# Optimization experiments

Hardware: AMD Instinct MI355X
Metric: run time of the kernel (lower is better)

The kernel has to match this reference:

```python
import jax, jax.numpy as jnp
import numpy as np

B, T, E, H, D = 1, 2048, 1024, 16, 64  # H*D == E required by module


def setup_inputs() -> dict:
    key = jax.random.key(0)
    ks = jax.random.split(key, 9)
    s_in = (2.0 / E) ** 0.5
    return {
        "x": jax.random.normal(ks[0], (B, T, E), jnp.float32),
        "wq": jax.random.normal(ks[1], (H * D, E), jnp.float32) * E ** -0.5,
        "wk": jax.random.normal(ks[2], (H * D, E), jnp.float32) * E ** -0.5,
        "wv": jax.random.normal(ks[3], (H * D, E), jnp.float32) * E ** -0.5,
        "wr": jax.random.normal(ks[4], (H, E, T), jnp.float32) * s_in,
        "wvr": jax.random.normal(ks[5], (H * D, E), jnp.float32) * E ** -0.5,
        "wj": jax.random.normal(ks[6], (E, E), jnp.float32) * E ** -0.5,
        "gate": jnp.zeros((H, 3), jnp.float32),
        "wo": jax.random.normal(ks[7], (E, H * D), jnp.float32) * E ** -0.5,
    }


def reference(x, wq, wk, wv, wr, wvr, wj, gate, wo):
    Bx, Tx, Ex = x.shape
    Hh = wr.shape[0]
    Dd = wq.shape[0] // Hh
    scale = 1.0 / Dd ** 0.5
    neg = -jnp.inf
    mask = jnp.triu(jnp.ones((Tx, Tx), bool), 1)  # True above diagonal

    def heads(w):  # (B,T,H*D) -> (B,H,T,D)
        return (x @ w.T).reshape(Bx, Tx, Hh, Dd).transpose(0, 2, 1, 3)

    # --- branch 1: standard causal QKV attention ---
    q, k, v = heads(wq), heads(wk), heads(wv)
    qkv_attn = jnp.einsum('bhqd,bhkd->bhqk', q, k) * scale
    qkv_attn = jnp.where(mask, neg, qkv_attn)
    qkv_out = jnp.einsum('bhqk,bhkd->bhqd', jax.nn.softmax(qkv_attn, axis=-1), v)

    # --- branch 2: RRPRAM learned per-position scores ---
    rv = heads(wvr)
    r = jnp.einsum('bte,het->bht', x, wr[:, :, :Tx])  # (B,H,T) key scores
    r_attn = jnp.where(mask, neg, (r * scale)[:, :, None, :])  # (B,H,T,T)
    rrp_out = jnp.einsum('bhqk,bhkd->bhqd', jax.nn.softmax(r_attn, axis=-1), rv)

    # --- branch 3: Janus self-resonance ---
    echo = x @ wj.T            # (B,T,E)
    echo_back = echo @ wj      # F.linear(echo, wj.weight.T)
    scores = (x * echo_back).sum(-1) / Ex ** 0.5  # (B,T)
    j_attn = jnp.where(mask, neg, scores[:, :, None] * scores[:, None, :])  # (B,T,T)
    jA = jax.nn.softmax(j_attn, axis=-1)
    j_val = echo.reshape(Bx, Tx, Hh, Dd).transpose(0, 2, 1, 3)
    jan_out = jnp.einsum('bqk,bhkd->bhqd', jA, j_val)

    # --- gated combine + output proj ---
    g = jax.nn.softmax(gate, axis=-1)  # (H,3)
    out = (g[:, 0][None, :, None, None] * qkv_out
           + g[:, 1][None, :, None, None] * rrp_out
           + g[:, 2][None, :, None, None] * jan_out)
    out = out.transpose(0, 2, 1, 3).reshape(Bx, Tx, Hh * Dd)
    return out @ wo.T
```

## Files before the change

### kernel.cpp

```cpp
#include <hip/hip_runtime.h>
#include <cstddef>
#include <cstdint>

#define TT 2048
#define EE 1024
#define HH 16
#define NSP 4

typedef unsigned short ushort;
typedef unsigned int uint;
typedef __attribute__((ext_vector_type(8))) short short8;
typedef __attribute__((ext_vector_type(8))) _Float16 half8;
typedef __attribute__((ext_vector_type(4))) float f32x4;
typedef __attribute__((ext_vector_type(4))) ushort ushort4v;

__device__ __forceinline__ ushort f2bf(float f) {
  uint u = __builtin_bit_cast(uint, f);
  u = (u + 0x7FFFu + ((u >> 16) & 1u)) >> 16;
  return (ushort)u;
}
__device__ __forceinline__ float bf2f(ushort h) {
  return __builtin_bit_cast(float, (uint)h << 16);
}

__device__ __forceinline__ void async16(ushort* lds, const ushort* g) {
  __builtin_amdgcn_global_load_lds(
      reinterpret_cast<const __attribute__((address_space(1))) void*>(
          reinterpret_cast<uintptr_t>(g)),
      reinterpret_cast<__attribute__((address_space(3))) void*>(
          static_cast<unsigned int>(reinterpret_cast<uintptr_t>(lds))),
      16, 0, 0);
}

__global__ __launch_bounds__(256) void cvt_x_k(
    const float* __restrict__ in, ushort* __restrict__ obf,
    ushort* __restrict__ oh, float* __restrict__ snorm, int n) {
  if (blockIdx.x == 0) {
    for (int i = threadIdx.x; i < TT; i += 256) snorm[i] = 0.f;
  }
  int i = (blockIdx.x * 256 + threadIdx.x) * 4;
  if (i >= n) return;
  float4 v = *(const float4*)(in + i);
  ushort4v b, h;
  b.x = f2bf(v.x); b.y = f2bf(v.y); b.z = f2bf(v.z); b.w = f2bf(v.w);
  h.x = __builtin_bit_cast(ushort, (_Float16)v.x);
  h.y = __builtin_bit_cast(ushort, (_Float16)v.y);
  h.z = __builtin_bit_cast(ushort, (_Float16)v.z);
  h.w = __builtin_bit_cast(ushort, (_Float16)v.w);
  *(ushort4v*)(obf + i) = b;
  *(ushort4v*)(oh + i) = h;
}

__global__ __launch_bounds__(256) void cvt_w_k(
    const float* __restrict__ s0, const float* __restrict__ s1,
    const float* __restrict__ s2, const float* __restrict__ s3,
    const float* __restrict__ s4, const float* __restrict__ s5,
    ushort* __restrict__ d0, ushort* __restrict__ d1,
    ushort* __restrict__ d2, ushort* __restrict__ d3,
    ushort* __restrict__ d4, ushort* __restrict__ d5, int n) {
  const int which = blockIdx.y;
  const float* src; ushort* dst;
  switch (which) {
    case 0: src = s0; dst = d0; break;
    case 1: src = s1; dst = d1; break;
    case 2: src = s2; dst = d2; break;
    case 3: src = s3; dst = d3; break;
    case 4: src = s4; dst = d4; break;
    default: src = s5; dst = d5; break;
  }
  int i = (blockIdx.x * 256 + threadIdx.x) * 4;
  if (i >= n) return;
  float4 v = *(const float4*)(src + i);
  ushort4v o;
  if (which == 5) {
    o.x = __builtin_bit_cast(ushort, (_Float16)v.x);
    o.y = __builtin_bit_cast(ushort, (_Float16)v.y);
    o.z = __builtin_bit_cast(ushort, (_Float16)v.z);
    o.w = __builtin_bit_cast(ushort, (_Float16)v.w);
  } else {
    o.x = f2bf(v.x); o.y = f2bf(v.y); o.z = f2bf(v.z); o.w = f2bf(v.w);
  }
  *(ushort4v*)(dst + i) = o;
}

__global__ __launch_bounds__(256) void transpose_k(
    const float* __restrict__ in, float* __restrict__ outT, int M, int N)
{
  __shared__ float tile[32][33];
  const int bn = blockIdx.x * 32;
  const int bm = blockIdx.y * 32;
  const int tx = threadIdx.x & 31, ty = threadIdx.x >> 5;
#pragma unroll
  for (int i = 0; i < 32; i += 8)
    tile[ty + i][tx] = in[(size_t)(bm + ty + i) * N + bn + tx];
  __syncthreads();
#pragma unroll
  for (int i = 0; i < 32; i += 8)
    outT[(size_t)(bn + ty + i) * M + bm + tx] = tile[tx][ty + i];
}

__global__ __launch_bounds__(256) void proj5(
    const ushort* __restrict__ Abf, const ushort* __restrict__ Ah,
    const ushort* __restrict__ B0, const ushort* __restrict__ B1,
    const ushort* __restrict__ B2, const ushort* __restrict__ B3,
    const ushort* __restrict__ B4,
    ushort* __restrict__ C0, ushort* __restrict__ C1,
    ushort* __restrict__ C2, ushort* __restrict__ C3,
    ushort* __restrict__ C4, float* __restrict__ snorm,
    int M, int N, int K)
{
  const ushort* A; const ushort* B; ushort* C; int om;
  switch (blockIdx.z) {
    case 0: A = Abf; B = B0; C = C0; om = 1; break;
    case 1: A = Abf; B = B1; C = C1; om = 1; break;
    case 2: A = Abf; B = B2; C = C2; om = 2; break;
    case 3: A = Abf; B = B3; C = C3; om = 1; break;
    default: A = Ah; B = B4; C = C4; om = 3; break;
  }
  const bool f16 = (blockIdx.z == 4);
  __shared__ __align__(16) ushort As[2][128 * 64];
  __shared__ __align__(16) ushort Bs[2][128 * 64];
  const int tid = threadIdx.x;
  const int m0 = blockIdx.y * 128, n0 = blockIdx.x * 128;
  const int w = tid >> 6, lane = tid & 63;
  const int wr = w >> 1, wc = w & 1;
  const int lr = lane & 15, lk = lane >> 4;
  const int srow = lane >> 3;
  const int scol = ((lane & 7) ^ srow) * 8;
  const ushort* AgL = A + (size_t)(m0 + w * 32 + srow) * K + scol;
  const ushort* BgL = B + (size_t)(n0 + w * 32 + srow) * K + scol;
  const int sbase = (w * 32) * 64;
  const int s0 = (lk ^ (lr & 7)) * 8;
  f32x4 acc[4][4] = {};
  const int NT = K >> 6;
#pragma unroll
  for (int c = 0; c < 4; ++c) {
    async16(&As[0][sbase + c * 8 * 64], AgL + (size_t)c * 8 * K);
    async16(&Bs[0][sbase + c * 8 * 64], BgL + (size_t)c * 8 * K);
  }
  __syncthreads();
  for (int kt = 0; kt < NT; ++kt) {
    const int cur = kt & 1;
    if (kt + 1 < NT) {
      const int kn = (kt + 1) << 6;
#pragma unroll
      for (int c = 0; c < 4; ++c) {
        async16(&As[cur ^ 1][sbase + c * 8 * 64], AgL + (size_t)c * 8 * K + kn);
        async16(&Bs[cur ^ 1][sbase + c * 8 * 64], BgL + (size_t)c * 8 * K + kn);
      }
    }
    short8 a0[4], a1[4], b0[4], b1[4];
#pragma unroll
    for (int i = 0; i < 4; ++i) {
      const ushort* p = &As[cur][(wr * 64 + i * 16 + lr) * 64];
      a0[i] = *(const short8*)(p + s0);
      a1[i] = *(const short8*)(p + (s0 ^ 32));
    }
#pragma unroll
    for (int j = 0; j < 4; ++j) {
      const ushort* p = &Bs[cur][(wc * 64 + j * 16 + lr) * 64];
      b0[j] = *(const short8*)(p + s0);
      b1[j] = *(const short8*)(p + (s0 ^ 32));
    }
    if (f16) {
#pragma unroll
      for (int i = 0; i < 4; ++i)
#pragma unroll
        for (int j = 0; j < 4; ++j) {
          acc[i][j] = __builtin_amdgcn_mfma_f32_16x16x32_f16(
              __builtin_bit_cast(half8, a0[i]), __builtin_bit_cast(half8, b0[j]),
              acc[i][j], 0, 0, 0);
          acc[i][j] = __builtin_amdgcn_mfma_f32_16x16x32_f16(
              __builtin_bit_cast(half8, a1[i]), __builtin_bit_cast(half8, b1[j]),
              acc[i][j], 0, 0, 0);
        }
    } else {
#pragma unroll
      for (int i = 0; i < 4; ++i)
#pragma unroll
        for (int j = 0; j < 4; ++j) {
          acc[i][j] = __builtin_amdgcn_mfma_f32_16x16x32_bf16(
              a0[i], b0[j], acc[i][j], 0, 0, 0);
          acc[i][j] = __builtin_amdgcn_mfma_f32_16x16x32_bf16(
              a1[i], b1[j], acc[i][j], 0, 0, 0);
        }
    }
    __syncthreads();
  }
#pragma unroll
  for (int i = 0; i < 4; ++i)
#pragma unroll
    for (int r = 0; r < 4; ++r) {
      int row = m0 + wr * 64 + i * 16 + lk * 4 + r;
#pragma unroll
      for (int j = 0; j < 4; ++j) {
        int col = n0 + wc * 64 + j * 16 + lr;
        ushort v = f2bf(acc[i][j][r]);
        if (om == 1)
          C[((size_t)(col >> 6) * M + row) * 64 + (col & 63)] = v;
        else if (om == 2)
          C[(size_t)(col >> 6) * 64 * M + (size_t)(col & 63) * M + row] = v;
        else
          C[(size_t)col * M + row] = v;
      }
    }
  if (om == 3) {
#pragma unroll
    for (int i = 0; i < 4; ++i)
#pragma unroll
      for (int r = 0; r < 4; ++r) {
        float p = 0.f;
#pragma unroll
        for (int j = 0; j < 4; ++j) p += acc[i][j][r] * acc[i][j][r];
        p += __shfl_xor(p, 1); p += __shfl_xor(p, 2);
        p += __shfl_xor(p, 4); p += __shfl_xor(p, 8);
        if (lr == 0)
          atomicAdd(&snorm[m0 + wr * 64 + i * 16 + lk * 4 + r], p);
      }
  }
}

template<bool CZ>
__global__ __launch_bounds__(256) void gemm_mfma(
    const ushort* __restrict__ A, const ushort* __restrict__ B,
    float* __restrict__ Cp, int M, int N, int K)
{
  __shared__ __align__(16) ushort As[2][128 * 64];
  __shared__ __align__(16) ushort Bs[2][128 * 64];
  const int tid = threadIdx.x;
  const int m0 = blockIdx.y * 128, n0 = blockIdx.x * 128;
  const int w = tid >> 6, lane = tid & 63;
  const int wr = w >> 1, wc = w & 1;
  const int lr = lane & 15, lk = lane >> 4;
  const int srow = lane >> 3;
  const int scol = ((lane & 7) ^ srow) * 8;
  const ushort* AgL = A + (size_t)(m0 + w * 32 + srow) * K + scol;
  const ushort* BgL = B + (size_t)(n0 + w * 32 + srow) * K + scol;
  const int sbase = (w * 32) * 64;
  const int s0 = (lk ^ (lr & 7)) * 8;
  f32x4 acc[4][4] = {};
  const int Keff = CZ ? (K < m0 + 128 ? K : m0 + 128) : K;
  const int NT = Keff >> 6;
#pragma unroll
  for (int c = 0; c < 4; ++c) {
    async16(&As[0][sbase + c * 8 * 64], AgL + (size_t)c * 8 * K);
    async16(&Bs[0][sbase + c * 8 * 64], BgL + (size_t)c * 8 * K);
  }
  __syncthreads();
  for (int kt = 0; kt < NT; ++kt) {
    const int cur = kt & 1;
    if (kt + 1 < NT) {
      const int kn = (kt + 1) << 6;
#pragma unroll
      for (int c = 0; c < 4; ++c) {
        async16(&As[cur ^ 1][sbase + c * 8 * 64], AgL + (size_t)c * 8 * K + kn);
        async16(&Bs[cur ^ 1][sbase + c * 8 * 64], BgL + (size_t)c * 8 * K + kn);
      }
    }
    short8 a0[4], a1[4], b0[4], b1[4];
#pragma unroll
    for (int i = 0; i < 4; ++i) {
      const ushort* p = &As[cur][(wr * 64 + i * 16 + lr) * 64];
      a0[i] = *(const short8*)(p + s0);
      a1[i] = *(const short8*)(p + (s0 ^ 32));
    }
#pragma unroll
    for (int j = 0; j < 4; ++j) {
      const ushort* p = &Bs[cur][(wc * 64 + j * 16 + lr) * 64];
      b0[j] = *(const short8*)(p + s0);
      b1[j] = *(const short8*)(p + (s0 ^ 32));
    }
#pragma unroll
    for (int i = 0; i < 4; ++i)
#pragma unroll
      for (int j = 0; j < 4; ++j) {
        acc[i][j] = __builtin_amdgcn_mfma_f32_16x16x32_bf16(
            a0[i], b0[j], acc[i][j], 0, 0, 0);
        acc[i][j] = __builtin_amdgcn_mfma_f32_16x16x32_bf16(
            a1[i], b1[j], acc[i][j], 0, 0, 0);
      }
    __syncthreads();
  }
#pragma unroll
  for (int i = 0; i < 4; ++i)
#pragma unroll
    for (int r = 0; r < 4; ++r) {
      int row = m0 + wr * 64 + i * 16 + lk * 4 + r;
#pragma unroll
      for (int j = 0; j < 4; ++j) {
        int col = n0 + wc * 64 + j * 16 + lr;
        Cp[(size_t)row * N + col] = acc[i][j][r];
      }
    }
}

__global__ __launch_bounds__(256) void flash_mfma(
    const ushort* __restrict__ Qg, const ushort* __restrict__ Kg,
    const ushort* __restrict__ Vg, float* __restrict__ pbuf, int T, int nqt)
{
  const int bid = blockIdx.x;
  const int xcd = bid & 7;
  const int jj = bid >> 3;
  const int h = xcd * 2 + (jj & 1);
  const int rest = jj >> 1;
  const int sp = rest & 3;
  const int qt = (nqt - 1) - (rest >> 2);
  const int q0 = qt * 64;
  const int nk = qt + 1;
  const int span = (nk + NSP - 1) >> 2;
  const int kb = sp * span;
  const int ke = (nk < kb + span) ? nk : (kb + span);
  const int tid = threadIdx.x, w = tid >> 6, lane = tid & 63;
  const int lr = lane & 15, lk = lane >> 4;
  const ushort* Q = Qg + (size_t)h * T * 64;
  const ushort* K = Kg + (size_t)h * T * 64;
  const ushort* V = Vg + (size_t)h * 64 * T;
  __shared__ __align__(16) ushort Ps[4][16 * 72];
  const float CEXP = 0.18033688f;

  f32x4 o[4] = {};
  float ls[4] = {0.f, 0.f, 0.f, 0.f};

  if (kb < ke) {
    short8 qa0 = *(const short8*)(Q + (size_t)(q0 + w * 16 + lr) * 64 + lk * 8);
    short8 qa1 = *(const short8*)(Q + (size_t)(q0 + w * 16 + lr) * 64 + 32 + lk * 8);
    short8 kb0[4], kb1[4];
#pragma unroll
    for (int c = 0; c < 4; ++c) {
      const ushort* kp = K + (size_t)(kb * 64 + c * 16 + lr) * 64 + lk * 8;
      kb0[c] = *(const short8*)kp;
      kb1[c] = *(const short8*)(kp + 32);
    }
    for (int kt = kb; kt < ke; ++kt) {
      const int k0 = kt * 64;
      short8 vb0[4], vb1[4];
#pragma unroll
      for (int c = 0; c < 4; ++c) {
        const ushort* vp = V + (size_t)(c * 16 + lr) * T + k0 + lk * 8;
        vb0[c] = *(const short8*)vp;
        vb1[c] = *(const short8*)(vp + 32);
      }
      f32x4 s[4];
      __builtin_amdgcn_s_setprio(1);
#pragma unroll
      for (int c = 0; c < 4; ++c) {
        f32x4 z = {};
        z = __builtin_amdgcn_mfma_f32_16x16x32_bf16(qa0, kb0[c], z, 0, 0, 0);
        z = __builtin_amdgcn_mfma_f32_16x16x32_bf16(qa1, kb1[c], z, 0, 0, 0);
        s[c] = z;
      }
      __builtin_amdgcn_s_setprio(0);
      if (kt + 1 < ke) {
#pragma unroll
        for (int c = 0; c < 4; ++c) {
          const ushort* kp = K + (size_t)(k0 + 64 + c * 16 + lr) * 64 + lk * 8;
          kb0[c] = *(const short8*)kp;
          kb1[c] = *(const short8*)(kp + 32);
        }
      }
      const bool diag = (kt == qt);
      const int rowbase = q0 + w * 16 + lk * 4;
#pragma unroll
      for (int c = 0; c < 4; ++c) {
        const int col = k0 + c * 16 + lr;
#pragma unroll
        for (int r = 0; r < 4; ++r) {
          float p = exp2f(s[c][r] * CEXP);
          if (diag && col > rowbase + r) p = 0.f;
          ls[r] += p;
          Ps[w][(lk * 4 + r) * 72 + c * 16 + lr] = f2bf(p);
        }
      }
      short8 pa0 = *(const short8*)(&Ps[w][lr * 72 + lk * 8]);
      short8 pa1 = *(const short8*)(&Ps[w][lr * 72 + 32 + lk * 8]);
      __builtin_amdgcn_s_setprio(1);
#pragma unroll
      for (int c = 0; c < 4; ++c) {
        o[c] = __builtin_amdgcn_mfma_f32_16x16x32_bf16(pa0, vb0[c], o[c], 0, 0, 0);
        o[c] = __builtin_amdgcn_mfma_f32_16x16x32_bf16(pa1, vb1[c], o[c], 0, 0, 0);
      }
      __builtin_amdgcn_s_setprio(0);
    }
#pragma unroll
    for (int r = 0; r < 4; ++r) {
      ls[r] += __shfl_xor(ls[r], 1);
      ls[r] += __shfl_xor(ls[r], 2);
      ls[r] += __shfl_xor(ls[r], 4);
      ls[r] += __shfl_xor(ls[r], 8);
    }
  }
  float* pb = pbuf + ((size_t)(h * nqt + qt) * NSP + sp) * 4160;
#pragma unroll
  for (int c = 0; c < 4; ++c)
#pragma unroll
    for (int r = 0; r < 4; ++r) {
      int row = w * 16 + lk * 4 + r;
      pb[(size_t)row * 64 + c * 16 + lr] = o[c][r];
    }
  if (lr == 0) {
#pragma unroll
    for (int r = 0; r < 4; ++r)
      pb[4096 + w * 16 + lk * 4 + r] = ls[r];
  }
}

__global__ __launch_bounds__(256) void flash_merge(
    const float* __restrict__ pbuf, ushort* __restrict__ O, int T, int nqt)
{
  const int b = blockIdx.x;
  const int h = b / nqt, qt = b - h * nqt;
  const float* p0 = pbuf + (size_t)b * NSP * 4160;
  const float* p1 = p0 + 4160;
  const float* p2 = p1 + 4160;
  const float* p3 = p2 + 4160;
  ushort* Oh = O + ((size_t)h * T + qt * 64) * 64;
  __shared__ float lsum[64];
  if (threadIdx.x < 64)
    lsum[threadIdx.x] = p0[4096 + threadIdx.x] + p1[4096 + threadIdx.x] +
                        p2[4096 + threadIdx.x] + p3[4096 + threadIdx.x];
  __syncthreads();
  for (int i = threadIdx.x; i < 4096; i += 256) {
    int r = i >> 6;
    Oh[i] = f2bf((p0[i] + p1[i] + p2[i] + p3[i]) / lsum[r]);
  }
}

__global__ __launch_bounds__(256) void rscore3(
    const float* __restrict__ xT, const float* __restrict__ wr,
    float* __restrict__ rpart, int T, int E)
{
  const int h = blockIdx.y;
  const int e0 = blockIdx.z * 64;
  const int t0 = (blockIdx.x * 256 + threadIdx.x) * 4;
  const float* wrh = wr + (size_t)h * E * T;
  float4 acc = {0.f, 0.f, 0.f, 0.f};
#pragma unroll 4
  for (int e = e0; e < e0 + 64; ++e) {
    float4 xv = *(const float4*)(xT + (size_t)e * T + t0);
    float4 wv = *(const float4*)(wrh + (size_t)e * T + t0);
    acc.x += xv.x * wv.x;
    acc.y += xv.y * wv.y;
    acc.z += xv.z * wv.z;
    acc.w += xv.w * wv.w;
  }
  *(float4*)(rpart + ((size_t)blockIdx.z * HH + h) * T + t0) = acc;
}

__global__ __launch_bounds__(256) void rsoftmax2(
    const float* __restrict__ rpart, float* __restrict__ w, int T)
{
  const int h = blockIdx.x;
  __shared__ float rs[TT];
  __shared__ float red[4];
  for (int t = threadIdx.x; t < T; t += 256) {
    float a = 0.f;
#pragma unroll
    for (int s = 0; s < 16; ++s) a += rpart[((size_t)s * HH + h) * T + t];
    rs[t] = a;
  }
  __syncthreads();
  float mx = -1e30f;
  for (int t = threadIdx.x; t < T; t += 256) mx = fmaxf(mx, rs[t]);
#pragma unroll
  for (int o = 32; o; o >>= 1) mx = fmaxf(mx, __shfl_xor(mx, o));
  if ((threadIdx.x & 63) == 0) red[threadIdx.x >> 6] = mx;
  __syncthreads();
  mx = fmaxf(fmaxf(red[0], red[1]), fmaxf(red[2], red[3]));
  float* wh = w + (size_t)h * T;
  for (int t = threadIdx.x; t < T; t += 256)
    wh[t] = __expf((rs[t] - mx) * 0.125f);
}

__global__ __launch_bounds__(64) void rrp_part(
    const float* __restrict__ wgt, const ushort* __restrict__ rv,
    float* __restrict__ segsum, int T)
{
  const int h = blockIdx.x, seg = blockIdx.y, d = threadIdx.x;
  const int segLen = T >> 5;
  const float* wh = wgt + (size_t)h * T;
  const ushort* rvh = rv + (size_t)h * T * 64;
  const int kbeg = seg * segLen, kend = kbeg + segLen;
  float num = 0.f, den = 0.f;
  for (int k = kbeg; k < kend; ++k) {
    float wk = wh[k];
    num += wk * bf2f(rvh[(size_t)k * 64 + d]);
    den += wk;
  }
  float* o = segsum + ((size_t)h * 32 + seg) * 65;
  o[d] = num;
  if (d == 0) o[64] = den;
}

__global__ __launch_bounds__(64) void rrp_scan2(
    const float* __restrict__ wgt, const ushort* __restrict__ rv,
    const float* __restrict__ segsum, ushort* __restrict__ out, int T)
{
  const int h = blockIdx.x, seg = blockIdx.y, d = threadIdx.x;
  const int segLen = T >> 5;
  const float* wh = wgt + (size_t)h * T;
  const ushort* rvh = rv + (size_t)h * T * 64;
  ushort* oh = out + (size_t)h * T * 64;
  float num = 0.f, den = 0.f;
  for (int s = 0; s < seg; ++s) {
    const float* p = segsum + ((size_t)h * 32 + s) * 65;
    num += p[d];
    den += p[64];
  }
  const int kbeg = seg * segLen, kend = kbeg + segLen;
  for (int k = kbeg; k < kend; ++k) {
    float wk = wh[k];
    num += wk * bf2f(rvh[(size_t)k * 64 + d]);
    den += wk;
    oh[(size_t)k * 64 + d] = f2bf(num / den);
  }
}

__global__ __launch_bounds__(256) void janus_w(
    const float* __restrict__ snorm, ushort* __restrict__ Wb,
    float* __restrict__ den, int T)
{
  const int q = blockIdx.x;
  const float sq = snorm[q] * 0.03125f;
  float mx = -1e30f;
  for (int k = threadIdx.x; k <= q; k += 256)
    mx = fmaxf(mx, sq * (snorm[k] * 0.03125f));
#pragma unroll
  for (int o = 32; o; o >>= 1) mx = fmaxf(mx, __shfl_xor(mx, o));
  __shared__ float red[4];
  if ((threadIdx.x & 63) == 0) red[threadIdx.x >> 6] = mx;
  __syncthreads();
  mx = fmaxf(fmaxf(red[0], red[1]), fmaxf(red[2], red[3]));
  float sum = 0.f;
  ushort* Wq = Wb + (size_t)q * T;
  for (int k = threadIdx.x; k < T; k += 256) {
    float wv = (k <= q) ? __expf(sq * (snorm[k] * 0.03125f) - mx) : 0.f;
    ushort wb = f2bf(wv);
    Wq[k] = wb;
    sum += bf2f(wb);
  }
#pragma unroll
  for (int o = 32; o; o >>= 1) sum += __shfl_xor(sum, o);
  __syncthreads();
  if ((threadIdx.x & 63) == 0) red[threadIdx.x >> 6] = sum;
  __syncthreads();
  if (threadIdx.x == 0) den[q] = red[0] + red[1] + red[2] + red[3];
}

__global__ __launch_bounds__(256) void combine_kernel(
    const ushort* __restrict__ a1, const ushort* __restrict__ a2,
    const float* __restrict__ jraw, const float* __restrict__ denj,
    const float* __restrict__ gate, ushort* __restrict__ comb, int T)
{
  const int idx = blockIdx.x * 256 + threadIdx.x;
  const int t = idx >> 10;
  const int c = idx & 1023;
  const int h = c >> 6;
  const int d = c & 63;
  float g0 = gate[h * 3 + 0], g1 = gate[h * 3 + 1], g2 = gate[h * 3 + 2];
  float mg = fmaxf(g0, fmaxf(g1, g2));
  float e0 = __expf(g0 - mg), e1 = __expf(g1 - mg), e2 = __expf(g2 - mg);
  float inv = 1.f / (e0 + e1 + e2);
  const size_t hd = ((size_t)h * T + t) * 64 + d;
  float v = (e0 * bf2f(a1[hd]) + e1 * bf2f(a2[hd]) + e2 * jraw[idx] / denj[t]) * inv;
  comb[idx] = f2bf(v);
}

extern "C" void kernel_launch(void* const* d_in, const int* in_sizes, int n_in,
                              void* d_out, int out_size, void* d_ws, size_t ws_size,
                              hipStream_t stream)
{
  (void)in_sizes; (void)n_in; (void)out_size; (void)ws_size;
  const float* x    = (const float*)d_in[0];
  const float* wq   = (const float*)d_in[1];
  const float* wk   = (const float*)d_in[2];
  const float* wv   = (const float*)d_in[3];
  const float* wr   = (const float*)d_in[4];
  const float* wvr  = (const float*)d_in[5];
  const float* wj   = (const float*)d_in[6];
  const float* gate = (const float*)d_in[7];
  const float* wo   = (const float*)d_in[8];
  float* out = (float*)d_out;

  const int T = TT, E = EE, H = HH;
  const int nqt = T / 64;
  const size_t TE = (size_t)T * E;
  const size_t EE2 = (size_t)E * E;
  const size_t TT2 = (size_t)T * T;

  ushort* u = (ushort*)d_ws;
  ushort* xbf   = u;
  ushort* xh    = xbf + TE;
  ushort* wqb   = xh + TE;
  ushort* wkb   = wqb + EE2;
  ushort* wvb   = wkb + EE2;
  ushort* wvrb  = wvb + EE2;
  ushort* wob   = wvrb + EE2;
  ushort* wjh   = wob + EE2;
  ushort* qhb   = wjh + EE2;
  ushort* khb   = qhb + TE;
  ushort* vtb   = khb + TE;
  ushort* rvhb  = vtb + TE;
  ushort* echoT = rvhb + TE;
  ushort* a1b   = echoT + TE;
  ushort* a2b   = a1b + TE;
  ushort* Wbf   = a2b + TE;
  ushort* combb = Wbf + TT2;
  float* jraw   = (float*)(combb + TE);
  float* wwb    = jraw + TE;
  float* snorm  = wwb + (size_t)H * T;
  float* denj   = snorm + T;
  float* rpart  = denj + T;
  float* segsum = rpart + (size_t)16 * H * T;
  float* xT     = segsum + (size_t)H * 32 * 65;
  float* pbuf   = xT + TE;

  dim3 blk(256);
  cvt_x_k<<<(int)(TE / 1024), blk, 0, stream>>>(x, xbf, xh, snorm, (int)TE);
  cvt_w_k<<<dim3((int)(EE2 / 1024), 6), blk, 0, stream>>>(
      wq, wk, wv, wvr, wo, wj, wqb, wkb, wvb, wvrb, wob, wjh, (int)EE2);
  transpose_k<<<dim3(E / 32, T / 32), blk, 0, stream>>>(x, xT, T, E);

  proj5<<<dim3(E / 128, T / 128, 5), blk, 0, stream>>>(
      xbf, xh, wqb, wkb, wvb, wvrb, wjh,
      qhb, khb, vtb, rvhb, echoT, snorm, T, E, E);

  rscore3<<<dim3(T / 1024, H, 16), blk, 0, stream>>>(xT, wr, rpart, T, E);
  rsoftmax2<<<H, blk, 0, stream>>>(rpart, wwb, T);

  flash_mfma<<<dim3(H * nqt * NSP), blk, 0, stream>>>(qhb, khb, vtb, pbuf, T, nqt);
  flash_merge<<<H * nqt, blk, 0, stream>>>(pbuf, a1b, T, nqt);

  rrp_part<<<dim3(H, 32), dim3(64), 0, stream>>>(wwb, rvhb, segsum, T);
  rrp_scan2<<<dim3(H, 32), dim3(64), 0, stream>>>(wwb, rvhb, segsum, a2b, T);

  janus_w<<<T, blk, 0, stream>>>(snorm, Wbf, denj, T);
  gemm_mfma<true><<<dim3(E / 128, T / 128), blk, 0, stream>>>(
      Wbf, echoT, jraw, T, E, T);

  combine_kernel<<<(int)(TE / 256), blk, 0, stream>>>(a1b, a2b, jraw, denj,
                                                      gate, combb, T);
  gemm_mfma<false><<<dim3(E / 128, T / 128), blk, 0, stream>>>(
      combb, wob, (float*)out, T, E, E);
}
```

Measured before the change: 459.6 us.

## Split flash attention blocks into single-wave blocks and prefetch V tiles

The flash attention kernel now launches one 64-thread wave per block instead of four waves per block, so each 16-row slice of a query tile is scheduled independently and the shared P staging buffer becomes per-block. V tiles for the next key step are now loaded a step ahead into a second register set, the same way K already was, so V load latency can overlap the current step's MFMA and exp work. The extra prefetch registers may lower occupancy. The four waves of a query tile no longer share a CU, which can reduce L2 and cache reuse of K and V.

```diff
diff --git a/kernel.cpp b/kernel.cpp
--- a/kernel.cpp
+++ b/kernel.cpp
@@ -294,28 +294,28 @@
     }
 }
 
-__global__ __launch_bounds__(256) void flash_mfma(
+__global__ __launch_bounds__(64) void flash_mfma(
     const ushort* __restrict__ Qg, const ushort* __restrict__ Kg,
     const ushort* __restrict__ Vg, float* __restrict__ pbuf, int T, int nqt)
 {
   const int bid = blockIdx.x;
   const int xcd = bid & 7;
-  const int jj = bid >> 3;
-  const int h = xcd * 2 + (jj & 1);
-  const int rest = jj >> 1;
-  const int sp = rest & 3;
-  const int qt = (nqt - 1) - (rest >> 2);
+  const int ii = bid >> 3;
+  const int h = xcd * 2 + (ii & 1);
+  const int sp = (ii >> 1) & 3;
+  const int w  = (ii >> 3) & 3;
+  const int qt = (nqt - 1) - (ii >> 5);
   const int q0 = qt * 64;
   const int nk = qt + 1;
   const int span = (nk + NSP - 1) >> 2;
   const int kb = sp * span;
   const int ke = (nk < kb + span) ? nk : (kb + span);
-  const int tid = threadIdx.x, w = tid >> 6, lane = tid & 63;
+  const int lane = threadIdx.x & 63;
   const int lr = lane & 15, lk = lane >> 4;
   const ushort* Q = Qg + (size_t)h * T * 64;
   const ushort* K = Kg + (size_t)h * T * 64;
   const ushort* V = Vg + (size_t)h * 64 * T;
-  __shared__ __align__(16) ushort Ps[4][16 * 72];
+  __shared__ __align__(16) ushort Ps[16 * 72];
   const float CEXP = 0.18033688f;
 
   f32x4 o[4] = {};
@@ -324,22 +324,18 @@
   if (kb < ke) {
     short8 qa0 = *(const short8*)(Q + (size_t)(q0 + w * 16 + lr) * 64 + lk * 8);
     short8 qa1 = *(const short8*)(Q + (size_t)(q0 + w * 16 + lr) * 64 + 32 + lk * 8);
-    short8 kb0[4], kb1[4];
+    short8 kb0[4], kb1[4], vb0[4], vb1[4], vn0[4], vn1[4];
 #pragma unroll
     for (int c = 0; c < 4; ++c) {
       const ushort* kp = K + (size_t)(kb * 64 + c * 16 + lr) * 64 + lk * 8;
       kb0[c] = *(const short8*)kp;
       kb1[c] = *(const short8*)(kp + 32);
+      const ushort* vp = V + (size_t)(c * 16 + lr) * T + kb * 64 + lk * 8;
+      vb0[c] = *(const short8*)vp;
+      vb1[c] = *(const short8*)(vp + 32);
     }
     for (int kt = kb; kt < ke; ++kt) {
       const int k0 = kt * 64;
-      short8 vb0[4], vb1[4];
-#pragma unroll
-      for (int c = 0; c < 4; ++c) {
-        const ushort* vp = V + (size_t)(c * 16 + lr) * T + k0 + lk * 8;
-        vb0[c] = *(const short8*)vp;
-        vb1[c] = *(const short8*)(vp + 32);
-      }
       f32x4 s[4];
       __builtin_amdgcn_s_setprio(1);
 #pragma unroll
@@ -356,6 +352,9 @@
           const ushort* kp = K + (size_t)(k0 + 64 + c * 16 + lr) * 64 + lk * 8;
           kb0[c] = *(const short8*)kp;
           kb1[c] = *(const short8*)(kp + 32);
+          const ushort* vp = V + (size_t)(c * 16 + lr) * T + k0 + 64 + lk * 8;
+          vn0[c] = *(const short8*)vp;
+          vn1[c] = *(const short8*)(vp + 32);
         }
       }
       const bool diag = (kt == qt);
@@ -368,11 +367,11 @@
           float p = exp2f(s[c][r] * CEXP);
           if (diag && col > rowbase + r) p = 0.f;
           ls[r] += p;
-          Ps[w][(lk * 4 + r) * 72 + c * 16 + lr] = f2bf(p);
+          Ps[(lk * 4 + r) * 72 + c * 16 + lr] = f2bf(p);
         }
       }
-      short8 pa0 = *(const short8*)(&Ps[w][lr * 72 + lk * 8]);
-      short8 pa1 = *(const short8*)(&Ps[w][lr * 72 + 32 + lk * 8]);
+      short8 pa0 = *(const short8*)(&Ps[lr * 72 + lk * 8]);
+      short8 pa1 = *(const short8*)(&Ps[lr * 72 + 32 + lk * 8]);
       __builtin_amdgcn_s_setprio(1);
 #pragma unroll
       for (int c = 0; c < 4; ++c) {
@@ -380,6 +379,13 @@
         o[c] = __builtin_amdgcn_mfma_f32_16x16x32_bf16(pa1, vb1[c], o[c], 0, 0, 0);
       }
       __builtin_amdgcn_s_setprio(0);
+      if (kt + 1 < ke) {
+#pragma unroll
+        for (int c = 0; c < 4; ++c) {
+          vb0[c] = vn0[c];
+          vb1[c] = vn1[c];
+        }
+      }
     }
 #pragma unroll
     for (int r = 0; r < 4; ++r) {
@@ -627,7 +633,8 @@
   rscore3<<<dim3(T / 1024, H, 16), blk, 0, stream>>>(xT, wr, rpart, T, E);
   rsoftmax2<<<H, blk, 0, stream>>>(rpart, wwb, T);
 
-  flash_mfma<<<dim3(H * nqt * NSP), blk, 0, stream>>>(qhb, khb, vtb, pbuf, T, nqt);
+  flash_mfma<<<dim3(H * nqt * NSP * 4), dim3(64), 0, stream>>>(
+      qhb, khb, vtb, pbuf, T, nqt);
   flash_merge<<<H * nqt, blk, 0, stream>>>(pbuf, a1b, T, nqt);
 
   rrp_part<<<dim3(H, 32), dim3(64), 0, stream>>>(wwb, rvhb, segsum, T);
```

Result: no change. 455.0 us (-1.0%).
